# Optimization experiments

Hardware: AMD Instinct MI355X
Metric: run time of the kernel (lower is better)

The kernel has to match this reference:

```python
import jax, jax.numpy as jnp
import numpy as np

NUM_EMBEDDINGS = 8192
EMBEDDING_DIM = 256
BETA = 0.25


def setup_inputs() -> dict:
    key = jax.random.key(0)
    k1, k2 = jax.random.split(key)
    z = jax.random.normal(k1, (16, 256, 32, 32), dtype=jnp.float32)
    # nn.Embedding weight init: uniform(-1/K, 1/K)
    emb = jax.random.uniform(k2, (NUM_EMBEDDINGS, EMBEDDING_DIM), dtype=jnp.float32,
                             minval=-1.0 / NUM_EMBEDDINGS, maxval=1.0 / NUM_EMBEDDINGS)
    return {"z": z, "emb": emb}


def reference(z, emb):
    b, c, h, w = z.shape
    flat = z.transpose(0, 2, 3, 1).reshape(-1, c)  # [B*H*W, C]
    distances = (jnp.sum(flat * flat, axis=1, keepdims=True)
                 - 2.0 * flat @ emb.T
                 + jnp.sum(emb * emb, axis=1))  # [B*H*W, K]
    indices = jnp.argmin(distances, axis=1)  # [B*H*W]
    quantized = emb[indices].reshape(b, h, w, c).transpose(0, 3, 1, 2)  # [B,C,H,W]
    codebook_loss = jnp.mean((jax.lax.stop_gradient(quantized) - z) ** 2)
    commitment_loss = BETA * jnp.mean((quantized - jax.lax.stop_gradient(z)) ** 2)
    quantized_st = z + jax.lax.stop_gradient(quantized - z)  # straight-through
    return quantized_st, codebook_loss, commitment_loss, indices.reshape(b, h, w)
```

## Files before the change

### kernel.cpp

```cpp
#include <hip/hip_runtime.h>

#define NROWS   16384
#define KCODES  8192
#define CDIM    256
#define HWS     1024
#define BSTRIDE 262144

#define WS_AN   0
#define WS_CE   16384
#define WS_CD   24576
#define WS_CI   90112
#define WS_IDX  155648
#define WS_LOSS 172032

__global__ void rownorm_z_k(const float* __restrict__ z, float* __restrict__ An) {
#pragma clang fp contract(off)
  int n = blockIdx.x * 256 + threadIdx.x;
  const float* base = z + ((size_t)(n >> 10)) * BSTRIDE + (n & 1023);
  float hs[2];
  for (int h = 0; h < 2; ++h) {
    float r[8];
#pragma unroll
    for (int j = 0; j < 8; ++j) { float v = base[(size_t)(h * 128 + j) * HWS]; r[j] = v * v; }
    for (int m = 1; m < 16; ++m) {
#pragma unroll
      for (int j = 0; j < 8; ++j) { float v = base[(size_t)(h * 128 + m * 8 + j) * HWS]; r[j] += v * v; }
    }
    hs[h] = ((r[0] + r[1]) + (r[2] + r[3])) + ((r[4] + r[5]) + (r[6] + r[7]));
  }
  An[n] = hs[0] + hs[1];
}

__global__ void rownorm_e_k(const float* __restrict__ emb, float* __restrict__ Ce) {
#pragma clang fp contract(off)
  int n = blockIdx.x * 256 + threadIdx.x;
  const float* base = emb + (size_t)n * CDIM;
  float hs[2];
  for (int h = 0; h < 2; ++h) {
    float r[8];
#pragma unroll
    for (int j = 0; j < 8; ++j) { float v = base[h * 128 + j]; r[j] = v * v; }
    for (int m = 1; m < 16; ++m) {
#pragma unroll
      for (int j = 0; j < 8; ++j) { float v = base[h * 128 + m * 8 + j]; r[j] += v * v; }
    }
    hs[h] = ((r[0] + r[1]) + (r[2] + r[3])) + ((r[4] + r[5]) + (r[6] + r[7]));
  }
  Ce[n] = hs[0] + hs[1];
}

__global__ void __launch_bounds__(256)
vq_argmin_k(const float* __restrict__ z, const float* __restrict__ emb,
            const float* __restrict__ An, const float* __restrict__ Ce,
            float* __restrict__ cand_d, int* __restrict__ cand_i) {
  __shared__ float As[32 * 20];
  __shared__ float Bs[16 * 132];
  __shared__ float redd[32 * 32];
  __shared__ int   redi[32 * 32];

  const int t  = threadIdx.x;
  const int tx = t & 31;
  const int ty = t >> 5;
  const int tile  = blockIdx.x >> 2;
  const int slice = blockIdx.x & 3;
  const int rbase = tile * 32;
  const int k0    = slice * 2048;

  const float* zb = z + ((size_t)(rbase >> 10)) * BSTRIDE + (rbase & 1023);

  float A_reg[4];
#pragma unroll
  for (int ri = 0; ri < 4; ++ri) A_reg[ri] = An[rbase + ty * 4 + ri];

  float best[4];
  int   bidx[4];
#pragma unroll
  for (int ri = 0; ri < 4; ++ri) { best[ri] = 3.4028235e38f; bidx[ri] = 0; }

  float acc[4][4];
#pragma unroll
  for (int ri = 0; ri < 4; ++ri)
#pragma unroll
    for (int ki = 0; ki < 4; ++ki) acc[ri][ki] = 0.f;

  const int a_c  = t >> 4;
  const int a_hw = (t & 15) * 2;
  const int b_ks = t >> 2;
  const int b_cp = (t & 3) * 4;

  const int iters = 16 * (2048 / 128);
  for (int it = 0; it < iters; ++it) {
    const int cc = it & 15;
    const int kb = k0 + (it >> 4) * 128;

    const float2 pa = *(const float2*)(zb + (size_t)(cc * 16 + a_c) * HWS + a_hw);
    const float4 pb0 = *(const float4*)(emb + (size_t)(kb + b_ks) * CDIM + cc * 16 + b_cp);
    const float4 pb1 = *(const float4*)(emb + (size_t)(kb + b_ks + 64) * CDIM + cc * 16 + b_cp);

    __syncthreads();
    As[(a_hw + 0) * 20 + a_c] = pa.x;
    As[(a_hw + 1) * 20 + a_c] = pa.y;
    Bs[(b_cp + 0) * 132 + b_ks] = pb0.x;
    Bs[(b_cp + 1) * 132 + b_ks] = pb0.y;
    Bs[(b_cp + 2) * 132 + b_ks] = pb0.z;
    Bs[(b_cp + 3) * 132 + b_ks] = pb0.w;
    Bs[(b_cp + 0) * 132 + b_ks + 64] = pb1.x;
    Bs[(b_cp + 1) * 132 + b_ks + 64] = pb1.y;
    Bs[(b_cp + 2) * 132 + b_ks + 64] = pb1.z;
    Bs[(b_cp + 3) * 132 + b_ks + 64] = pb1.w;
    __syncthreads();

#pragma unroll
    for (int g = 0; g < 4; ++g) {
      const float4 b0 = *(const float4*)&Bs[(g * 4 + 0) * 132 + tx * 4];
      const float4 b1 = *(const float4*)&Bs[(g * 4 + 1) * 132 + tx * 4];
      const float4 b2 = *(const float4*)&Bs[(g * 4 + 2) * 132 + tx * 4];
      const float4 b3 = *(const float4*)&Bs[(g * 4 + 3) * 132 + tx * 4];
#pragma unroll
      for (int ri = 0; ri < 4; ++ri) {
        const float4 a = *(const float4*)&As[(ty * 4 + ri) * 20 + g * 4];
        acc[ri][0] = fmaf(a.x, b0.x, fmaf(a.y, b1.x, fmaf(a.z, b2.x, fmaf(a.w, b3.x, acc[ri][0]))));
        acc[ri][1] = fmaf(a.x, b0.y, fmaf(a.y, b1.y, fmaf(a.z, b2.y, fmaf(a.w, b3.y, acc[ri][1]))));
        acc[ri][2] = fmaf(a.x, b0.z, fmaf(a.y, b1.z, fmaf(a.z, b2.z, fmaf(a.w, b3.z, acc[ri][2]))));
        acc[ri][3] = fmaf(a.x, b0.w, fmaf(a.y, b1.w, fmaf(a.z, b2.w, fmaf(a.w, b3.w, acc[ri][3]))));
      }
    }

    if (cc == 15) {
      const int kk = kb + tx * 4;
      const float4 ce = *(const float4*)&Ce[kk];
#pragma unroll
      for (int ri = 0; ri < 4; ++ri) {
        const float Ar = A_reg[ri];
        const float d0 = (Ar - 2.0f * acc[ri][0]) + ce.x;
        const float d1 = (Ar - 2.0f * acc[ri][1]) + ce.y;
        const float d2 = (Ar - 2.0f * acc[ri][2]) + ce.z;
        const float d3 = (Ar - 2.0f * acc[ri][3]) + ce.w;
        if (d0 < best[ri]) { best[ri] = d0; bidx[ri] = kk; }
        if (d1 < best[ri]) { best[ri] = d1; bidx[ri] = kk + 1; }
        if (d2 < best[ri]) { best[ri] = d2; bidx[ri] = kk + 2; }
        if (d3 < best[ri]) { best[ri] = d3; bidx[ri] = kk + 3; }
        acc[ri][0] = 0.f; acc[ri][1] = 0.f; acc[ri][2] = 0.f; acc[ri][3] = 0.f;
      }
    }
  }

#pragma unroll
  for (int ri = 0; ri < 4; ++ri) {
    redd[(ty * 4 + ri) * 32 + tx] = best[ri];
    redi[(ty * 4 + ri) * 32 + tx] = bidx[ri];
  }
  __syncthreads();
  if (t < 32) {
    float bd = redd[t * 32];
    int   bi = redi[t * 32];
    for (int j = 1; j < 32; ++j) {
      const float d  = redd[t * 32 + j];
      const int   i2 = redi[t * 32 + j];
      if (d < bd || (d == bd && i2 < bi)) { bd = d; bi = i2; }
    }
    const int n = rbase + t;
    cand_d[n * 4 + slice] = bd;
    cand_i[n * 4 + slice] = bi;
  }
}

__global__ void vq_merge_k(const float* __restrict__ cand_d, const int* __restrict__ cand_i,
                           int* __restrict__ idx_final, float* __restrict__ idxf_out) {
  const int n = blockIdx.x * 256 + threadIdx.x;
  float bd = cand_d[n * 4];
  int   bi = cand_i[n * 4];
#pragma unroll
  for (int s = 1; s < 4; ++s) {
    const float d  = cand_d[n * 4 + s];
    const int   i2 = cand_i[n * 4 + s];
    if (d < bd || (d == bd && i2 < bi)) { bd = d; bi = i2; }
  }
  idx_final[n] = bi;
  idxf_out[n] = (float)bi;
}

__launch_bounds__(256)
__global__ void vq_gather_loss_k(const float* __restrict__ z, const float* __restrict__ emb,
                                 const int* __restrict__ idx_final,
                                 float* __restrict__ qout, float* __restrict__ loss_acc) {
  __shared__ float Qs[32 * 260];
  __shared__ int   kidx[32];
  __shared__ float warp_s[4];
  const int t = threadIdx.x;
  const int rbase = blockIdx.x * 32;
  if (t < 32) kidx[t] = idx_final[rbase + t];
  __syncthreads();
  {
    const int r = t >> 3, cp = t & 7;
    const float4* er = (const float4*)(emb + (size_t)kidx[r] * CDIM);
#pragma unroll
    for (int j = 0; j < 8; ++j) {
      const int c4 = cp + j * 8;
      const float4 v = er[c4];
      *(float4*)&Qs[r * 260 + c4 * 4] = v;
    }
  }
  __syncthreads();
  const int b = rbase >> 10, hw0 = rbase & 1023;
  const float* zb = z + (size_t)b * BSTRIDE + hw0;
  float* qb = qout + (size_t)b * BSTRIDE + hw0;
  float s = 0.f;
  const int hwl = t & 31, cg = t >> 5;
  for (int i = 0; i < 32; ++i) {
    const int c = cg * 32 + i;
    const float q  = Qs[hwl * 260 + c];
    const size_t off = (size_t)c * HWS + hwl;
    const float zv = zb[off];
    const float d  = q - zv;
    qb[off] = zv + d;
    s += d * d;
  }
  for (int off = 32; off; off >>= 1) s += __shfl_down(s, off, 64);
  if ((t & 63) == 0) warp_s[t >> 6] = s;
  __syncthreads();
  if (t == 0) atomicAdd(loss_acc, warp_s[0] + warp_s[1] + warp_s[2] + warp_s[3]);
}

__global__ void vq_finalize_k(const float* __restrict__ loss_acc, float* __restrict__ out_loss) {
  const float m = loss_acc[0] * (1.0f / 4194304.0f);
  out_loss[0] = m;
  out_loss[1] = 0.25f * m;
}

extern "C" void kernel_launch(void* const* d_in, const int* in_sizes, int n_in,
                              void* d_out, int out_size, void* d_ws, size_t ws_size,
                              hipStream_t stream) {
  (void)in_sizes; (void)n_in; (void)out_size; (void)ws_size;
  const float* z   = (const float*)d_in[0];
  const float* emb = (const float*)d_in[1];
  float* out      = (float*)d_out;
  float* q_out    = out;
  float* loss_out = out + 4194304;
  float* idxf_out = out + 4194306;

  float* ws       = (float*)d_ws;
  float* An       = ws + WS_AN;
  float* Ce       = ws + WS_CE;
  float* cand_d   = ws + WS_CD;
  int*   cand_i   = (int*)(ws + WS_CI);
  int*   idx_fin  = (int*)(ws + WS_IDX);
  float* loss_acc = ws + WS_LOSS;

  hipMemsetAsync(loss_acc, 0, sizeof(float), stream);
  rownorm_z_k<<<64, 256, 0, stream>>>(z, An);
  rownorm_e_k<<<32, 256, 0, stream>>>(emb, Ce);
  vq_argmin_k<<<2048, 256, 0, stream>>>(z, emb, An, Ce, cand_d, cand_i);
  vq_merge_k<<<64, 256, 0, stream>>>(cand_d, cand_i, idx_fin, idxf_out);
  vq_gather_loss_k<<<512, 256, 0, stream>>>(z, emb, idx_fin, q_out, loss_acc);
  vq_finalize_k<<<1, 1, 0, stream>>>(loss_acc, loss_out);
}
```

Measured before the change: 1.086 ms.

## Reshape argmin tile to 64 rows by 64 codes with register prefetch

The distance/argmin kernel now uses a 64-row by 64-code block tile instead of 32 by 128, which halves the grid and changes the shared-memory layouts. It also software-prefetches the next global loads into registers before the compute phase, so load latency overlaps with the FMAs. The intent is to cut redundant codebook reads per row and hide global latency. In exchange, the smaller code width may cost some B reuse, and the restructured indexing could introduce subtle address bugs.

```diff
diff --git a/kernel.cpp b/kernel.cpp
--- a/kernel.cpp
+++ b/kernel.cpp
@@ -53,17 +53,17 @@
 vq_argmin_k(const float* __restrict__ z, const float* __restrict__ emb,
             const float* __restrict__ An, const float* __restrict__ Ce,
             float* __restrict__ cand_d, int* __restrict__ cand_i) {
-  __shared__ float As[32 * 20];
-  __shared__ float Bs[16 * 132];
-  __shared__ float redd[32 * 32];
-  __shared__ int   redi[32 * 32];
+  __shared__ float As[64 * 20];
+  __shared__ float Bs[16 * 68];
+  __shared__ float redd[64 * 16];
+  __shared__ int   redi[64 * 16];
 
   const int t  = threadIdx.x;
-  const int tx = t & 31;
-  const int ty = t >> 5;
+  const int tx = t & 15;
+  const int ty = t >> 4;
   const int tile  = blockIdx.x >> 2;
   const int slice = blockIdx.x & 3;
-  const int rbase = tile * 32;
+  const int rbase = tile * 64;
   const int k0    = slice * 2048;
 
   const float* zb = z + ((size_t)(rbase >> 10)) * BSTRIDE + (rbase & 1023);
@@ -83,51 +83,58 @@
 #pragma unroll
     for (int ki = 0; ki < 4; ++ki) acc[ri][ki] = 0.f;
 
-  const int a_c  = t >> 4;
-  const int a_hw = (t & 15) * 2;
-  const int b_ks = t >> 2;
-  const int b_cp = (t & 3) * 4;
-
-  const int iters = 16 * (2048 / 128);
-  for (int it = 0; it < iters; ++it) {
-    const int cc = it & 15;
-    const int kb = k0 + (it >> 4) * 128;
-
-    const float2 pa = *(const float2*)(zb + (size_t)(cc * 16 + a_c) * HWS + a_hw);
-    const float4 pb0 = *(const float4*)(emb + (size_t)(kb + b_ks) * CDIM + cc * 16 + b_cp);
-    const float4 pb1 = *(const float4*)(emb + (size_t)(kb + b_ks + 64) * CDIM + cc * 16 + b_cp);
-
-    __syncthreads();
-    As[(a_hw + 0) * 20 + a_c] = pa.x;
-    As[(a_hw + 1) * 20 + a_c] = pa.y;
-    Bs[(b_cp + 0) * 132 + b_ks] = pb0.x;
-    Bs[(b_cp + 1) * 132 + b_ks] = pb0.y;
-    Bs[(b_cp + 2) * 132 + b_ks] = pb0.z;
-    Bs[(b_cp + 3) * 132 + b_ks] = pb0.w;
-    Bs[(b_cp + 0) * 132 + b_ks + 64] = pb1.x;
-    Bs[(b_cp + 1) * 132 + b_ks + 64] = pb1.y;
-    Bs[(b_cp + 2) * 132 + b_ks + 64] = pb1.z;
-    Bs[(b_cp + 3) * 132 + b_ks + 64] = pb1.w;
-    __syncthreads();
-
-#pragma unroll
-    for (int g = 0; g < 4; ++g) {
-      const float4 b0 = *(const float4*)&Bs[(g * 4 + 0) * 132 + tx * 4];
-      const float4 b1 = *(const float4*)&Bs[(g * 4 + 1) * 132 + tx * 4];
-      const float4 b2 = *(const float4*)&Bs[(g * 4 + 2) * 132 + tx * 4];
-      const float4 b3 = *(const float4*)&Bs[(g * 4 + 3) * 132 + tx * 4];
-#pragma unroll
-      for (int ri = 0; ri < 4; ++ri) {
-        const float4 a = *(const float4*)&As[(ty * 4 + ri) * 20 + g * 4];
-        acc[ri][0] = fmaf(a.x, b0.x, fmaf(a.y, b1.x, fmaf(a.z, b2.x, fmaf(a.w, b3.x, acc[ri][0]))));
-        acc[ri][1] = fmaf(a.x, b0.y, fmaf(a.y, b1.y, fmaf(a.z, b2.y, fmaf(a.w, b3.y, acc[ri][1]))));
-        acc[ri][2] = fmaf(a.x, b0.z, fmaf(a.y, b1.z, fmaf(a.z, b2.z, fmaf(a.w, b3.z, acc[ri][2]))));
-        acc[ri][3] = fmaf(a.x, b0.w, fmaf(a.y, b1.w, fmaf(a.z, b2.w, fmaf(a.w, b3.w, acc[ri][3]))));
+  const int a_c   = t >> 4;
+  const int a_hw  = (t & 15) * 4;
+  const int b_cd  = t >> 2;
+  const int b_cp  = (t & 3) * 4;
+
+  const float* pAb = zb + (size_t)a_c * HWS + a_hw;
+  const float* pBb = emb + (size_t)(k0 + b_cd) * CDIM + b_cp;
+
+  float4 pa = *(const float4*)(pAb);
+  float4 pb = *(const float4*)(pBb);
+
+  const float* pB = pBb;
+  for (int kc = 0; kc < 32; ++kc) {
+#pragma unroll 4
+    for (int cc = 0; cc < 16; ++cc) {
+      __syncthreads();
+      As[(a_hw + 0) * 20 + a_c] = pa.x;
+      As[(a_hw + 1) * 20 + a_c] = pa.y;
+      As[(a_hw + 2) * 20 + a_c] = pa.z;
+      As[(a_hw + 3) * 20 + a_c] = pa.w;
+      Bs[(b_cp + 0) * 68 + b_cd] = pb.x;
+      Bs[(b_cp + 1) * 68 + b_cd] = pb.y;
+      Bs[(b_cp + 2) * 68 + b_cd] = pb.z;
+      Bs[(b_cp + 3) * 68 + b_cd] = pb.w;
+      __syncthreads();
+
+      {
+        const int ncc = (cc + 1) & 15;
+        pa = *(const float4*)(pAb + (size_t)ncc * (16 * HWS));
+        const float* nB = (cc == 15) ? ((kc == 31) ? pBb : pB + 64 * CDIM) : pB;
+        pb = *(const float4*)(nB + ncc * 16);
       }
-    }
-
-    if (cc == 15) {
-      const int kk = kb + tx * 4;
+
+#pragma unroll
+      for (int g = 0; g < 4; ++g) {
+        const float4 b0 = *(const float4*)&Bs[(g * 4 + 0) * 68 + tx * 4];
+        const float4 b1 = *(const float4*)&Bs[(g * 4 + 1) * 68 + tx * 4];
+        const float4 b2 = *(const float4*)&Bs[(g * 4 + 2) * 68 + tx * 4];
+        const float4 b3 = *(const float4*)&Bs[(g * 4 + 3) * 68 + tx * 4];
+#pragma unroll
+        for (int ri = 0; ri < 4; ++ri) {
+          const float4 a = *(const float4*)&As[(ty * 4 + ri) * 20 + g * 4];
+          acc[ri][0] = fmaf(a.x, b0.x, fmaf(a.y, b1.x, fmaf(a.z, b2.x, fmaf(a.w, b3.x, acc[ri][0]))));
+          acc[ri][1] = fmaf(a.x, b0.y, fmaf(a.y, b1.y, fmaf(a.z, b2.y, fmaf(a.w, b3.y, acc[ri][1]))));
+          acc[ri][2] = fmaf(a.x, b0.z, fmaf(a.y, b1.z, fmaf(a.z, b2.z, fmaf(a.w, b3.z, acc[ri][2]))));
+          acc[ri][3] = fmaf(a.x, b0.w, fmaf(a.y, b1.w, fmaf(a.z, b2.w, fmaf(a.w, b3.w, acc[ri][3]))));
+        }
+      }
+    }
+
+    {
+      const int kk = k0 + kc * 64 + tx * 4;
       const float4 ce = *(const float4*)&Ce[kk];
 #pragma unroll
       for (int ri = 0; ri < 4; ++ri) {
@@ -143,20 +150,21 @@
         acc[ri][0] = 0.f; acc[ri][1] = 0.f; acc[ri][2] = 0.f; acc[ri][3] = 0.f;
       }
     }
+    pB += 64 * CDIM;
   }
 
 #pragma unroll
   for (int ri = 0; ri < 4; ++ri) {
-    redd[(ty * 4 + ri) * 32 + tx] = best[ri];
-    redi[(ty * 4 + ri) * 32 + tx] = bidx[ri];
-  }
-  __syncthreads();
-  if (t < 32) {
-    float bd = redd[t * 32];
-    int   bi = redi[t * 32];
-    for (int j = 1; j < 32; ++j) {
-      const float d  = redd[t * 32 + j];
-      const int   i2 = redi[t * 32 + j];
+    redd[(ty * 4 + ri) * 16 + tx] = best[ri];
+    redi[(ty * 4 + ri) * 16 + tx] = bidx[ri];
+  }
+  __syncthreads();
+  if (t < 64) {
+    float bd = redd[t * 16];
+    int   bi = redi[t * 16];
+    for (int j = 1; j < 16; ++j) {
+      const float d  = redd[t * 16 + j];
+      const int   i2 = redi[t * 16 + j];
       if (d < bd || (d == bd && i2 < bi)) { bd = d; bi = i2; }
     }
     const int n = rbase + t;
@@ -250,7 +258,7 @@
   hipMemsetAsync(loss_acc, 0, sizeof(float), stream);
   rownorm_z_k<<<64, 256, 0, stream>>>(z, An);
   rownorm_e_k<<<32, 256, 0, stream>>>(emb, Ce);
-  vq_argmin_k<<<2048, 256, 0, stream>>>(z, emb, An, Ce, cand_d, cand_i);
+  vq_argmin_k<<<1024, 256, 0, stream>>>(z, emb, An, Ce, cand_d, cand_i);
   vq_merge_k<<<64, 256, 0, stream>>>(cand_d, cand_i, idx_fin, idxf_out);
   vq_gather_loss_k<<<512, 256, 0, stream>>>(z, emb, idx_fin, q_out, loss_acc);
   vq_finalize_k<<<1, 1, 0, stream>>>(loss_acc, loss_out);
```

Measured after the change: 1.121 ms. +3.2%, slower.
